# Kernel optimization log

Hardware: AMD Instinct MI355X
Metric: run time of the kernel (lower is better)

## Reference

```python
import jax, jax.numpy as jnp
import numpy as np

B, DIN, DOUT, E = 131072, 512, 512, 16


def setup_inputs() -> dict:
    key = jax.random.key(0)
    k_x, k_wg, k_we = jax.random.split(key, 3)
    x = jax.random.normal(k_x, (B, DIN), dtype=jnp.float32)
    # gating network params
    Wg = jax.random.normal(k_wg, (DIN, E), dtype=jnp.float32) * 0.02
    bg = jnp.zeros((E,), dtype=jnp.float32)
    # GRN params (torch inits them to zero -> GRN is identity at init)
    gamma = jnp.zeros((E,), dtype=jnp.float32)
    beta = jnp.zeros((E,), dtype=jnp.float32)
    # per-expert linear params, stacked [E, DIN, DOUT]
    We = jax.random.normal(k_we, (E, DIN, DOUT), dtype=jnp.float32) * 0.02
    be = jnp.zeros((E, DOUT), dtype=jnp.float32)
    return {"x": x, "Wg": Wg, "bg": bg, "gamma": gamma, "beta": beta,
            "We": We, "be": be, "topk": 2}


def reference(x, Wg, bg, gamma, beta, We, be, topk):
    # ---- gating: linear -> GRN over expert dim -> softmax ----
    logits = x @ Wg + bg                                   # [B, E]
    Gx = jnp.linalg.norm(logits, axis=1, keepdims=True)    # [B, 1] L2 over experts
    Nx = Gx / (jnp.mean(Gx, axis=0, keepdims=True) + 1e-6) # [B, 1]
    logits = gamma * (logits * Nx) + beta + logits         # GRN residual
    gates = jax.nn.softmax(logits, axis=-1)                # [B, E]
    # ---- top-k routing ----
    top_vals, top_idx = jax.lax.top_k(gates, topk)         # [B, k]
    n_tok = x.shape[0]
    # combine weights scattered back to dense [B, E] (zero for unrouted experts)
    w = jnp.zeros_like(gates).at[jnp.arange(n_tok)[:, None], top_idx].add(top_vals)
    # ---- per-expert linear + weighted combine ----
    out = jnp.zeros((n_tok, We.shape[-1]), dtype=x.dtype)
    for e in range(We.shape[0]):  # small fixed loop over experts
        out = out + w[:, e:e + 1] * (x @ We[e] + be[e])
    return out
```

## Files before the change

kernel.cpp:

```cpp
#include <hip/hip_runtime.h>
#include <hip/hip_bf16.h>
#include <stdint.h>

#define NTOK 131072
#define NE 16

typedef __attribute__((ext_vector_type(8))) short short8;
typedef __attribute__((ext_vector_type(4))) float f32x4;

#define AS1 __attribute__((address_space(1)))
#define AS3 __attribute__((address_space(3)))

__device__ __forceinline__ ushort f2bf(float f) {
    __hip_bfloat16 h = __float2bfloat16(f);
    return *reinterpret_cast<ushort*>(&h);
}


__global__ void k_init(int* ctrl) {
    int tid = threadIdx.x;
    if (tid < 144) ctrl[tid] = 0;
}

__global__ __launch_bounds__(256) void k_wet(const float* __restrict__ We, ushort* __restrict__ WeT) {
    __shared__ float t[64][65];
    int e = blockIdx.z, k0 = blockIdx.x * 64, n0 = blockIdx.y * 64;
    int tid = threadIdx.x;
    const float* src = We + ((size_t)e * 512 + k0) * 512 + n0;
    #pragma unroll
    for (int i = 0; i < 16; i++) {
        int idx = i * 256 + tid;
        int r = idx >> 6, c = idx & 63;
        t[r][c] = src[(size_t)r * 512 + c];
    }
    __syncthreads();
    ushort* dst = WeT + ((size_t)e * 512 + n0) * 512 + k0;
    #pragma unroll
    for (int i = 0; i < 16; i++) {
        int idx = i * 256 + tid;
        int rn = idx >> 6, ck = idx & 63;
        dst[(size_t)rn * 512 + ck] = f2bf(t[ck][rn]);
    }
}

__global__ __launch_bounds__(256) void k_gate(const float* __restrict__ x, const float* __restrict__ Wg,
                                              const float* __restrict__ bg, float* __restrict__ logits,
                                              float* __restrict__ partials, ushort* __restrict__ xbf) {
    __shared__ float WgL[512 * 16];
    __shared__ float xs[256][33];
    __shared__ float wsum[4];
    const int tid = threadIdx.x;
    #pragma unroll
    for (int i = 0; i < 32; i++) WgL[i * 256 + tid] = Wg[i * 256 + tid];
    const size_t tokBase = (size_t)blockIdx.x * 256;
    float acc[16];
    #pragma unroll
    for (int e = 0; e < 16; e++) acc[e] = 0.f;

    for (int kc = 0; kc < 16; kc++) {
        __syncthreads();
        #pragma unroll
        for (int i = 0; i < 8; i++) {
            int idx = (i << 8) + tid;
            int rr = idx >> 3, cq = (idx & 7) << 2;
            const float4 v = *(const float4*)&x[(tokBase + rr) * 512 + (kc << 5) + cq];
            xs[rr][cq] = v.x; xs[rr][cq + 1] = v.y; xs[rr][cq + 2] = v.z; xs[rr][cq + 3] = v.w;
            if (xbf) {
                ushort4 uw;
                uw.x = f2bf(v.x); uw.y = f2bf(v.y); uw.z = f2bf(v.z); uw.w = f2bf(v.w);
                *(ushort4*)&xbf[(tokBase + rr) * 512 + (kc << 5) + cq] = uw;
            }
        }
        __syncthreads();
        #pragma unroll
        for (int j = 0; j < 32; j++) {
            float xv = xs[tid][j];
            const float* wr = &WgL[((kc << 5) + j) << 4];
            #pragma unroll
            for (int e = 0; e < 16; e++) acc[e] = fmaf(xv, wr[e], acc[e]);
        }
    }

    float lg[16];
    float ss = 0.f;
    #pragma unroll
    for (int e = 0; e < 16; e++) {
        float v = acc[e] + bg[e];
        lg[e] = v;
        ss += v * v;
    }
    float gx = sqrtf(ss);
    float r = gx;
    #pragma unroll
    for (int off = 32; off >= 1; off >>= 1) r += __shfl_down(r, off);
    if ((tid & 63) == 0) wsum[tid >> 6] = r;
    __syncthreads();
    if (tid == 0) partials[blockIdx.x] = wsum[0] + wsum[1] + wsum[2] + wsum[3];
    float4* lo = (float4*)(logits + (tokBase + tid) * 16);
    lo[0] = make_float4(lg[0], lg[1], lg[2], lg[3]);
    lo[1] = make_float4(lg[4], lg[5], lg[6], lg[7]);
    lo[2] = make_float4(lg[8], lg[9], lg[10], lg[11]);
    lo[3] = make_float4(lg[12], lg[13], lg[14], lg[15]);
}

__global__ void k_redsum(const float* __restrict__ partials, float* __restrict__ sumGx) {
    int tid = threadIdx.x;
    float s = 0.f;
    #pragma unroll
    for (int i = 0; i < 8; i++) s += partials[tid + i * 64];
    #pragma unroll
    for (int off = 32; off >= 1; off >>= 1) s += __shfl_down(s, off);
    if (tid == 0) *sumGx = s;
}

__global__ __launch_bounds__(256) void k_route(const float* __restrict__ logits, const float* __restrict__ gamma,
                                               const float* __restrict__ beta, const float* __restrict__ sumGx,
                                               int* __restrict__ eP, float2* __restrict__ wP,
                                               int* __restrict__ cnts, int* __restrict__ blockHist) {
    __shared__ int h[32];
    int tid = threadIdx.x;
    if (tid < 32) h[tid] = 0;
    __syncthreads();
    float mean = sumGx[0] * (1.0f / 131072.0f);
    float inv_mean = 1.0f / (mean + 1e-6f);
    #pragma unroll
    for (int it = 0; it < 4; it++) {
        size_t t = (size_t)blockIdx.x * 1024 + it * 256 + tid;
        const float4* lr = (const float4*)(logits + t * 16);
        float4 a0 = lr[0], a1 = lr[1], a2 = lr[2], a3 = lr[3];
        float lg[16] = {a0.x, a0.y, a0.z, a0.w, a1.x, a1.y, a1.z, a1.w,
                        a2.x, a2.y, a2.z, a2.w, a3.x, a3.y, a3.z, a3.w};
        float ss = 0.f;
        #pragma unroll
        for (int e = 0; e < 16; e++) ss += lg[e] * lg[e];
        float nx = sqrtf(ss) * inv_mean;
        #pragma unroll
        for (int e = 0; e < 16; e++) lg[e] = gamma[e] * (lg[e] * nx) + beta[e] + lg[e];
        int e1 = 0; float v1 = lg[0];
        #pragma unroll
        for (int e = 1; e < 16; e++) if (lg[e] > v1) { v1 = lg[e]; e1 = e; }
        int e2 = -1; float v2 = -3.4e38f;
        #pragma unroll
        for (int e = 0; e < 16; e++) if (e != e1 && lg[e] > v2) { v2 = lg[e]; e2 = e; }
        float s = 0.f;
        #pragma unroll
        for (int e = 0; e < 16; e++) s += expf(lg[e] - v1);
        float w1 = 1.0f / s;
        float w2 = expf(v2 - v1) / s;
        eP[t] = e1 | (e2 << 8);
        wP[t] = make_float2(w1, w2);
        atomicAdd(&h[e1], 1);
        atomicAdd(&h[16 + e2], 1);
    }
    __syncthreads();
    if (tid < 32) {
        atomicAdd(&cnts[tid], h[tid]);
        blockHist[blockIdx.x * 32 + tid] = h[tid];
    }
}

__global__ void k_scan(int* ctrl, int* blockHist) {
    int t = threadIdx.x;
    if (t < 32) {
        int run = 0;
        for (int b = 0; b < 128; b++) {
            int v = blockHist[b * 32 + t];
            blockHist[b * 32 + t] = run;
            run += v;
        }
    }
    __syncthreads();
    if (t == 0) {
        int s = 0;
        for (int e = 0; e < 16; e++) { ctrl[64 + e] = s; s += ctrl[e]; }
        s = 0;
        for (int e = 0; e < 16; e++) { ctrl[80 + e] = s; s += ctrl[16 + e]; }
        int tt = 0; ctrl[96] = 0;
        for (int e = 0; e < 16; e++) { tt += (ctrl[e] + 63) >> 6; ctrl[96 + e + 1] = tt; }
        tt = 0; ctrl[113] = 0;
        for (int e = 0; e < 16; e++) { tt += (ctrl[16 + e] + 63) >> 6; ctrl[113 + e + 1] = tt; }
    }
}

__global__ __launch_bounds__(256) void k_scatter(const int* __restrict__ eP, const float2* __restrict__ wP,
                                                 const int* __restrict__ ctrl, const int* __restrict__ blockHist,
                                                 int* __restrict__ listA, float* __restrict__ wA,
                                                 int* __restrict__ listB, float* __restrict__ wB) {
    __shared__ int waveCnt[4][32];
    __shared__ int runCnt[32];
    const int tid = threadIdx.x;
    const int lane = tid & 63;
    const int wv = tid >> 6;
    if (tid < 32) runCnt[tid] = blockHist[blockIdx.x * 32 + tid];
    __syncthreads();
    const unsigned long long below = (1ull << lane) - 1ull;
    for (int it = 0; it < 4; it++) {
        size_t t = (size_t)blockIdx.x * 1024 + it * 256 + tid;
        int ep = eP[t];
        float2 w = wP[t];
        int e1 = ep & 255, e2 = (ep >> 8) & 255;
        int r1 = 0, r2 = 0;
        for (int e = 0; e < 16; e++) {
            unsigned long long m1 = __ballot(e1 == e);
            unsigned long long m2 = __ballot(e2 == e);
            if (e1 == e) r1 = __popcll(m1 & below);
            if (e2 == e) r2 = __popcll(m2 & below);
            if (lane == e) {
                waveCnt[wv][e] = __popcll(m1);
                waveCnt[wv][16 + e] = __popcll(m2);
            }
        }
        __syncthreads();
        if (tid < 32) {
            int s = runCnt[tid];
            #pragma unroll
            for (int ww = 0; ww < 4; ww++) { int v = waveCnt[ww][tid]; waveCnt[ww][tid] = s; s += v; }
            runCnt[tid] = s;
        }
        __syncthreads();
        int i1 = ctrl[64 + e1] + waveCnt[wv][e1] + r1;
        listA[i1] = (int)t; wA[i1] = w.x;
        int i2 = ctrl[80 + e2] + waveCnt[wv][16 + e2] + r2;
        listB[i2] = (int)t; wB[i2] = w.y;
        __syncthreads();
    }
}

template <int ADD, int ABF>
__global__ __launch_bounds__(512, 2) void k_gemm(const float* __restrict__ x, const ushort* __restrict__ xbf,
                                                 const ushort* __restrict__ WeT,
                                                 const float* __restrict__ be,
                                                 const int* __restrict__ list, const float* __restrict__ wlist,
                                                 const int* __restrict__ cnts, const int* __restrict__ offs,
                                                 const int* __restrict__ tileOff,
                                                 float* __restrict__ out) {
    __shared__ alignas(16) ushort lds[36864];
    const int tid = threadIdx.x;
    const int q = (int)gridDim.x >> 3;
    const int ry = ((int)blockIdx.x & 7) * q + ((int)blockIdx.x >> 3);
    if (ry >= tileOff[16]) return;
    int e = 0;
    #pragma unroll
    for (int i = 1; i < 16; i++) if (ry >= tileOff[i]) e = i;
    const int cnt = cnts[e];
    const int off = offs[e];
    const int rowStart = (ry - tileOff[e]) << 6;

    const int sRow = tid >> 3, sQ = tid & 7;
    const int gRow = rowStart + sRow;
    const int tokS = (gRow < cnt) ? list[off + gRow] : 0;
    const float* xrowF = x + (size_t)tokS * 512 + sQ * 8;
    const ushort* xrowH = xbf + (size_t)tokS * 512 + sQ * 8;
    const int aswz = (sRow & 7) << 4;
    const int awr0 = 65536 + sRow * 128;

    const char* weB = (const char*)WeT + (size_t)e * 524288;

    const int lane = tid & 63;
    const int wid = tid >> 6;
    const int wN = wid << 6;
    const int l16 = lane & 15;
    const int lq = lane >> 4;
    const int mswz = (l16 & 7) << 4;
    const int kbL = lq << 4;

    f32x4 acc[4][4];
    f32x4 zero = {0.f, 0.f, 0.f, 0.f};
    #pragma unroll
    for (int i = 0; i < 4; i++)
        #pragma unroll
        for (int j = 0; j < 4; j++) acc[i][j] = zero;

    auto stageB = [&](int kt) {
        #pragma unroll
        for (int i = 0; i < 8; i++) {
            int D = (tid << 4) + (i << 13);
            int nr = D >> 7, inner = D & 127;
            int sb = inner ^ ((nr & 7) << 4);
            const char* gp = weB + nr * 1024 + kt * 128 + sb;
            __builtin_amdgcn_global_load_lds((const AS1 void*)gp, (AS3 void*)&lds[D >> 1], 16, 0, 0);
        }
    };
    float4 vaF[2];
    short8 vaH;
    auto loadA = [&](int kt) {
        if (ABF) {
            vaH = *(const short8*)(xrowH + kt * 64);
        } else {
            const float4* xp = (const float4*)(xrowF + kt * 64);
            vaF[0] = xp[0]; vaF[1] = xp[1];
        }
    };
    auto writeA = [&]() {
        int db = awr0 + ((sQ << 4) ^ aswz);
        if (ABF) {
            *(short8*)((char*)lds + db) = vaH;
        } else {
            alignas(16) ushort tw[8];
            float4 p = vaF[0], q2 = vaF[1];
            tw[0] = f2bf(p.x); tw[1] = f2bf(p.y); tw[2] = f2bf(p.z); tw[3] = f2bf(p.w);
            tw[4] = f2bf(q2.x); tw[5] = f2bf(q2.y); tw[6] = f2bf(q2.z); tw[7] = f2bf(q2.w);
            *(short8*)((char*)lds + db) = *(const short8*)tw;
        }
    };
    auto compute = [&]() {
        #pragma unroll
        for (int ks = 0; ks < 2; ks++) {
            const int kb = (ks << 6) + kbL;
            short8 af[4], bfr[4];
            #pragma unroll
            for (int mf = 0; mf < 4; mf++) {
                int m = (mf << 4) + l16;
                af[mf] = *(const short8*)((const char*)lds + 65536 + (m << 7) + (kb ^ mswz));
            }
            #pragma unroll
            for (int nf = 0; nf < 4; nf++) {
                int n = wN + (nf << 4) + l16;
                bfr[nf] = *(const short8*)((const char*)lds + (n << 7) + (kb ^ mswz));
            }
            #pragma unroll
            for (int mf = 0; mf < 4; mf++)
                #pragma unroll
                for (int nf = 0; nf < 4; nf++)
                    acc[mf][nf] = __builtin_amdgcn_mfma_f32_16x16x32_bf16(af[mf], bfr[nf], acc[mf][nf], 0, 0, 0);
        }
    };

    loadA(0);
    #pragma unroll
    for (int kt = 0; kt < 8; kt++) {
        __syncthreads();
        stageB(kt);
        writeA();
        if (kt < 7) loadA(kt + 1);
        __syncthreads();
        compute();
    }

    float bias[4];
    #pragma unroll
    for (int nf = 0; nf < 4; nf++) bias[nf] = be[e * 512 + wN + (nf << 4) + l16];
    float* lsf = (float*)lds;
    __syncthreads();
    #pragma unroll
    for (int mf = 0; mf < 4; mf++) {
        int rb = rowStart + (mf << 4) + (lq << 2);
        #pragma unroll
        for (int i = 0; i < 4; i++) {
            int r = rb + i;
            float wv_ = (r < cnt) ? wlist[off + r] : 0.f;
            int lrow = (lq << 2) + i;
            #pragma unroll
            for (int nf = 0; nf < 4; nf++)
                lsf[lrow * 516 + wN + (nf << 4) + l16] = wv_ * (acc[mf][nf][i] + bias[nf]);
        }
        __syncthreads();
        {
            int lrow = tid >> 5, seg = tid & 31;
            int r = rowStart + (mf << 4) + lrow;
            if (r < cnt) {
                int tok = list[off + r];
                float* orow = out + (size_t)tok * 512;
                #pragma unroll
                for (int j = 0; j < 4; j++) {
                    int c = (seg << 2) + (j << 7);
                    float4 v = *(float4*)&lsf[lrow * 516 + c];
                    if (ADD) {
                        float4 o = *(const float4*)&orow[c];
                        v.x += o.x; v.y += o.y; v.z += o.z; v.w += o.w;
                    }
                    *(float4*)&orow[c] = v;
                }
            }
        }
        __syncthreads();
    }
}

extern "C" void kernel_launch(void* const* d_in, const int* in_sizes, int n_in,
                              void* d_out, int out_size, void* d_ws, size_t ws_size,
                              hipStream_t stream) {
    const float* x = (const float*)d_in[0];
    const float* Wg = (const float*)d_in[1];
    const float* bg = (const float*)d_in[2];
    const float* gamma = (const float*)d_in[3];
    const float* beta = (const float*)d_in[4];
    const float* We = (const float*)d_in[5];
    const float* be = (const float*)d_in[6];
    float* out = (float*)d_out;
    char* ws = (char*)d_ws;

    ushort* WeT = (ushort*)(ws);
    float* logits = (float*)(ws + 8388608);
    int* listA = (int*)(ws + 16777216);
    float* wA = (float*)(ws + 17301504);
    int* listB = (int*)(ws + 17825792);
    float* wB = (float*)(ws + 18350080);
    int* eP = (int*)(ws + 18874368);
    float2* wP = (float2*)(ws + 19398656);
    int* ctrl = (int*)(ws + 20447232);
    int* blockHist = (int*)(ws + 20451328);
    float* ctrlF = (float*)ctrl;
    float* partials = (float*)(ws + 16777216);

    const size_t XBF_OFF = 20480000;
    const size_t XBF_BYTES = (size_t)NTOK * 512 * 2;
    bool useBF = (ws_size >= XBF_OFF + XBF_BYTES);
    ushort* xbf = useBF ? (ushort*)(ws + XBF_OFF) : nullptr;

    k_init<<<1, 256, 0, stream>>>(ctrl);
    k_wet<<<dim3(8, 8, 16), 256, 0, stream>>>(We, WeT);
    k_gate<<<512, 256, 0, stream>>>(x, Wg, bg, logits, partials, xbf);
    k_redsum<<<1, 64, 0, stream>>>(partials, ctrlF + 130);
    k_route<<<128, 256, 0, stream>>>(logits, gamma, beta, ctrlF + 130, eP, wP, ctrl, blockHist);
    k_scan<<<1, 64, 0, stream>>>(ctrl, blockHist);
    k_scatter<<<128, 256, 0, stream>>>(eP, wP, ctrl, blockHist, listA, wA, listB, wB);
    if (useBF) {
        k_gemm<0, 1><<<2064, 512, 0, stream>>>(x, xbf, WeT, be, listA, wA, ctrl, ctrl + 64, ctrl + 96, out);
        k_gemm<1, 1><<<2064, 512, 0, stream>>>(x, xbf, WeT, be, listB, wB, ctrl + 16, ctrl + 80, ctrl + 113, out);
    } else {
        k_gemm<0, 0><<<2064, 512, 0, stream>>>(x, xbf, WeT, be, listA, wA, ctrl, ctrl + 64, ctrl + 96, out);
        k_gemm<1, 0><<<2064, 512, 0, stream>>>(x, xbf, WeT, be, listB, wB, ctrl + 16, ctrl + 80, ctrl + 113, out);
    }
}
```

Baseline: 523.6 us.

## Split GEMM tiles along N and double-buffer B staging with manual waitcnts

Each GEMM block now covers a 64x256 output tile instead of 64x512, so twice as many blocks are launched. The freed LDS holds two B buffers, and the next K-slice is prefetched via global_load_lds while the current one is computed, using explicit vmcnt/lgkmcnt waits and raw barriers. The epilogue writes all rows at once instead of four 16-row passes. The aim is to hide global-load latency and raise parallelism. The cost is that every A tile (gathered x rows) is loaded twice, plus more barriers per K step, and the hand-counted waits are fragile.

```diff
diff --git a/kernel.cpp b/kernel.cpp
--- a/kernel.cpp
+++ b/kernel.cpp
@@ -10,6 +10,13 @@
 
 #define AS1 __attribute__((address_space(1)))
 #define AS3 __attribute__((address_space(3)))
+
+#define WAIT_VMCNT(n) do { asm volatile("s_waitcnt vmcnt(" #n ")" ::: "memory"); \
+                           __builtin_amdgcn_sched_barrier(0); } while (0)
+#define WAIT_LGKM0    do { asm volatile("s_waitcnt lgkmcnt(0)" ::: "memory"); \
+                           __builtin_amdgcn_sched_barrier(0); } while (0)
+#define BAR()         do { asm volatile("s_barrier" ::: "memory"); \
+                           __builtin_amdgcn_sched_barrier(0); } while (0)
 
 __device__ __forceinline__ ushort f2bf(float f) {
     __hip_bfloat16 h = __float2bfloat16(f);
@@ -237,7 +244,9 @@
     __shared__ alignas(16) ushort lds[36864];
     const int tid = threadIdx.x;
     const int q = (int)gridDim.x >> 3;
-    const int ry = ((int)blockIdx.x & 7) * q + ((int)blockIdx.x >> 3);
+    const int bid = ((int)blockIdx.x & 7) * q + ((int)blockIdx.x >> 3);
+    const int ry = bid >> 1;
+    const int nh = bid & 1;
     if (ry >= tileOff[16]) return;
     int e = 0;
     #pragma unroll
@@ -245,6 +254,7 @@
     const int cnt = cnts[e];
     const int off = offs[e];
     const int rowStart = (ry - tileOff[e]) << 6;
+    const int n0 = nh << 8;
 
     const int sRow = tid >> 3, sQ = tid & 7;
     const int gRow = rowStart + sRow;
@@ -254,31 +264,33 @@
     const int aswz = (sRow & 7) << 4;
     const int awr0 = 65536 + sRow * 128;
 
-    const char* weB = (const char*)WeT + (size_t)e * 524288;
+    const char* weB = (const char*)WeT + (size_t)e * 524288 + (size_t)n0 * 1024;
 
     const int lane = tid & 63;
     const int wid = tid >> 6;
-    const int wN = wid << 6;
+    const int wM = (wid >> 2) << 5;
+    const int wN = (wid & 3) << 6;
     const int l16 = lane & 15;
     const int lq = lane >> 4;
     const int mswz = (l16 & 7) << 4;
     const int kbL = lq << 4;
 
-    f32x4 acc[4][4];
+    f32x4 acc[2][4];
     f32x4 zero = {0.f, 0.f, 0.f, 0.f};
     #pragma unroll
-    for (int i = 0; i < 4; i++)
+    for (int i = 0; i < 2; i++)
         #pragma unroll
         for (int j = 0; j < 4; j++) acc[i][j] = zero;
 
-    auto stageB = [&](int kt) {
-        #pragma unroll
-        for (int i = 0; i < 8; i++) {
+    auto stageB = [&](int kt, int buf) {
+        #pragma unroll
+        for (int i = 0; i < 4; i++) {
             int D = (tid << 4) + (i << 13);
             int nr = D >> 7, inner = D & 127;
             int sb = inner ^ ((nr & 7) << 4);
             const char* gp = weB + nr * 1024 + kt * 128 + sb;
-            __builtin_amdgcn_global_load_lds((const AS1 void*)gp, (AS3 void*)&lds[D >> 1], 16, 0, 0);
+            __builtin_amdgcn_global_load_lds((const AS1 void*)gp,
+                                             (AS3 void*)&lds[(buf * 32768 + D) >> 1], 16, 0, 0);
         }
     };
     float4 vaF[2];
@@ -303,23 +315,23 @@
             *(short8*)((char*)lds + db) = *(const short8*)tw;
         }
     };
-    auto compute = [&]() {
+    auto compute = [&](int buf) {
         #pragma unroll
         for (int ks = 0; ks < 2; ks++) {
             const int kb = (ks << 6) + kbL;
-            short8 af[4], bfr[4];
-            #pragma unroll
-            for (int mf = 0; mf < 4; mf++) {
-                int m = (mf << 4) + l16;
+            short8 af[2], bfr[4];
+            #pragma unroll
+            for (int mf = 0; mf < 2; mf++) {
+                int m = wM + (mf << 4) + l16;
                 af[mf] = *(const short8*)((const char*)lds + 65536 + (m << 7) + (kb ^ mswz));
             }
             #pragma unroll
             for (int nf = 0; nf < 4; nf++) {
                 int n = wN + (nf << 4) + l16;
-                bfr[nf] = *(const short8*)((const char*)lds + (n << 7) + (kb ^ mswz));
+                bfr[nf] = *(const short8*)((const char*)lds + buf * 32768 + (n << 7) + (kb ^ mswz));
             }
             #pragma unroll
-            for (int mf = 0; mf < 4; mf++)
+            for (int mf = 0; mf < 2; mf++)
                 #pragma unroll
                 for (int nf = 0; nf < 4; nf++)
                     acc[mf][nf] = __builtin_amdgcn_mfma_f32_16x16x32_bf16(af[mf], bfr[nf], acc[mf][nf], 0, 0, 0);
@@ -327,53 +339,66 @@
     };
 
     loadA(0);
+    stageB(0, 0);
+    writeA();
+    loadA(1);
+    WAIT_LGKM0;
+    BAR();
+
     #pragma unroll
     for (int kt = 0; kt < 8; kt++) {
-        __syncthreads();
-        stageB(kt);
-        writeA();
-        if (kt < 7) loadA(kt + 1);
-        __syncthreads();
-        compute();
+        const int buf = kt & 1;
+        if (kt < 7) stageB(kt + 1, buf ^ 1);
+        if (kt < 7) {
+            if (ABF) { WAIT_VMCNT(5); } else { WAIT_VMCNT(6); }
+        } else {
+            WAIT_VMCNT(0);
+        }
+        BAR();
+        compute(buf);
+        WAIT_LGKM0;
+        BAR();
+        if (kt < 7) writeA();
+        if (kt < 6) loadA(kt + 2);
+        WAIT_LGKM0;
+        BAR();
     }
 
     float bias[4];
     #pragma unroll
-    for (int nf = 0; nf < 4; nf++) bias[nf] = be[e * 512 + wN + (nf << 4) + l16];
+    for (int nf = 0; nf < 4; nf++) bias[nf] = be[e * 512 + n0 + wN + (nf << 4) + l16];
     float* lsf = (float*)lds;
     __syncthreads();
     #pragma unroll
-    for (int mf = 0; mf < 4; mf++) {
-        int rb = rowStart + (mf << 4) + (lq << 2);
+    for (int mf = 0; mf < 2; mf++) {
         #pragma unroll
         for (int i = 0; i < 4; i++) {
-            int r = rb + i;
+            int lrow = wM + (mf << 4) + (lq << 2) + i;
+            int r = rowStart + lrow;
             float wv_ = (r < cnt) ? wlist[off + r] : 0.f;
-            int lrow = (lq << 2) + i;
             #pragma unroll
             for (int nf = 0; nf < 4; nf++)
-                lsf[lrow * 516 + wN + (nf << 4) + l16] = wv_ * (acc[mf][nf][i] + bias[nf]);
-        }
-        __syncthreads();
-        {
-            int lrow = tid >> 5, seg = tid & 31;
-            int r = rowStart + (mf << 4) + lrow;
-            if (r < cnt) {
-                int tok = list[off + r];
-                float* orow = out + (size_t)tok * 512;
-                #pragma unroll
-                for (int j = 0; j < 4; j++) {
-                    int c = (seg << 2) + (j << 7);
-                    float4 v = *(float4*)&lsf[lrow * 516 + c];
-                    if (ADD) {
-                        float4 o = *(const float4*)&orow[c];
-                        v.x += o.x; v.y += o.y; v.z += o.z; v.w += o.w;
-                    }
-                    *(float4*)&orow[c] = v;
+                lsf[lrow * 260 + wN + (nf << 4) + l16] = wv_ * (acc[mf][nf][i] + bias[nf]);
+        }
+    }
+    __syncthreads();
+    {
+        int lrow = tid >> 3, seg = tid & 7;
+        int r = rowStart + lrow;
+        if (r < cnt) {
+            int tok = list[off + r];
+            float* orow = out + (size_t)tok * 512 + n0 + (seg << 5);
+            const float* lrowp = &lsf[lrow * 260 + (seg << 5)];
+            #pragma unroll
+            for (int j = 0; j < 8; j++) {
+                float4 v = *(const float4*)&lrowp[j << 2];
+                if (ADD) {
+                    float4 o = *(const float4*)&orow[j << 2];
+                    v.x += o.x; v.y += o.y; v.z += o.z; v.w += o.w;
                 }
+                *(float4*)&orow[j << 2] = v;
             }
         }
-        __syncthreads();
     }
 }
 
@@ -416,10 +441,10 @@
     k_scan<<<1, 64, 0, stream>>>(ctrl, blockHist);
     k_scatter<<<128, 256, 0, stream>>>(eP, wP, ctrl, blockHist, listA, wA, listB, wB);
     if (useBF) {
-        k_gemm<0, 1><<<2064, 512, 0, stream>>>(x, xbf, WeT, be, listA, wA, ctrl, ctrl + 64, ctrl + 96, out);
-        k_gemm<1, 1><<<2064, 512, 0, stream>>>(x, xbf, WeT, be, listB, wB, ctrl + 16, ctrl + 80, ctrl + 113, out);
+        k_gemm<0, 1><<<4128, 512, 0, stream>>>(x, xbf, WeT, be, listA, wA, ctrl, ctrl + 64, ctrl + 96, out);
+        k_gemm<1, 1><<<4128, 512, 0, stream>>>(x, xbf, WeT, be, listB, wB, ctrl + 16, ctrl + 80, ctrl + 113, out);
     } else {
-        k_gemm<0, 0><<<2064, 512, 0, stream>>>(x, xbf, WeT, be, listA, wA, ctrl, ctrl + 64, ctrl + 96, out);
-        k_gemm<1, 0><<<2064, 512, 0, stream>>>(x, xbf, WeT, be, listB, wB, ctrl + 16, ctrl + 80, ctrl + 113, out);
-    }
-}
+        k_gemm<0, 0><<<4128, 512, 0, stream>>>(x, xbf, WeT, be, listA, wA, ctrl, ctrl + 64, ctrl + 96, out);
+        k_gemm<1, 0><<<4128, 512, 0, stream>>>(x, xbf, WeT, be, listB, wB, ctrl + 16, ctrl + 80, ctrl + 113, out);
+    }
+}
```

Measured after the change: 588.4 us. +12.4%, slower.
